# Kernel optimization log

Hardware: AMD Instinct MI355X
Metric: run time of the kernel (lower is better)

Reference implementation:

```python
import jax, jax.numpy as jnp
import numpy as np

CHANNELS = 32


def _mlp(x, W1, b1, W2, b2, W3, b3):
    # FNN: Linear -> ReLU -> Linear -> ReLU -> Linear (last layer linear)
    h = jax.nn.relu(x @ W1 + b1)
    h = jax.nn.relu(h @ W2 + b2)
    return h @ W3 + b3


def setup_inputs() -> dict:
    key = jax.random.key(0)
    ks = jax.random.split(key, 8)
    E = 262144
    C = CHANNELS
    H = 128
    d_in = 4  # 2 * spatial_dim
    d_out = C * (C + 1)  # 1056
    s = lambda fan_in: 1.0 / np.sqrt(fan_in)
    return {
        "pos_i": jax.random.normal(ks[0], (E, 2), jnp.float32),
        "pos_j": jax.random.normal(ks[1], (E, 2), jnp.float32),
        "v_j": jax.random.normal(ks[2], (E, C), jnp.float32),
        "W1": jax.random.normal(ks[3], (d_in, H), jnp.float32) * s(d_in),
        "b1": jnp.zeros((H,), jnp.float32),
        "W2": jax.random.normal(ks[4], (H, H), jnp.float32) * s(H),
        "b2": jnp.zeros((H,), jnp.float32),
        "W3": jax.random.normal(ks[5], (H, d_out), jnp.float32) * s(H),
        "b3": jnp.zeros((d_out,), jnp.float32),
    }


def reference(pos_i, pos_j, v_j, W1, b1, W2, b2, W3, b3):
    C = CHANNELS
    pos_ij = jnp.concatenate((pos_i, pos_j), axis=-1)          # [E, 2*spatial_dim]
    kernel = _mlp(pos_ij, W1, b1, W2, b2, W3, b3)
    kernel = kernel.reshape(-1, C, C + 1)                      # [E, C, C+1]
    mat, bias = kernel[..., :, :-1], kernel[..., :, -1]        # [E,C,C], [E,C]
    return jnp.einsum('eij,ej->ei', mat, v_j) + bias           # [E, C]
```

## Files before the change

### kernel.cpp

```cpp
#include <hip/hip_runtime.h>


#define E_TOTAL 262144
#define EPB 256
#define NBLK (E_TOTAL / EPB)

typedef float f32x4 __attribute__((ext_vector_type(4)));
typedef short s8v  __attribute__((ext_vector_type(8)));
typedef unsigned int u32;

__device__ __forceinline__ unsigned short f2bf(float x) {
  unsigned u = __float_as_uint(x);
  u += 0x7fffu + ((u >> 16) & 1u);
  return (unsigned short)(u >> 16);
}

__device__ __forceinline__ void ld16_g2l(const void* g, void* l) {
  __builtin_amdgcn_global_load_lds((const __attribute__((address_space(1))) u32*)g,
                                   (__attribute__((address_space(3))) u32*)l, 16, 0, 0);
}

__global__ void prep_pack(const float* __restrict__ W2, const float* __restrict__ W3,
                          const float* __restrict__ b3,
                          unsigned short* __restrict__ Wg2, unsigned short* __restrict__ W2f,
                          unsigned short* __restrict__ b3f, float* __restrict__ b3c) {
  int idx = blockIdx.x * 256 + threadIdx.x;
  if (idx < 135168) {
    int k = idx / 1056, c = idx % 1056;
    int i = c / 33, jc = c % 33;
    int col = jc * 32 + i;
    int nnt = col >> 4, low = col & 15;
    int nn = (nnt & 1) ? (33 + (nnt >> 1)) : (nnt >> 1);
    int ks = k >> 5, kr = k & 31;
    int lane = ((kr >> 3) << 4) + low;
    int jj = k & 7;
    Wg2[((nn * 4 + ks) * 64 + lane) * 8 + jj] = f2bf(W3[idx]);
  }
  if (idx < 16384) {
    int k = idx >> 7, n = idx & 127;
    int ks = k >> 5, kr = k & 31;
    int nt = n >> 4, low = n & 15;
    int l = ((kr >> 3) << 4) + low;
    int jj = k & 7;
    W2f[((ks * 8 + nt) * 64 + l) * 8 + jj] = f2bf(W2[idx]);
  }
  if (idx < 1024) {
    int jj = idx & 7, lane = (idx >> 3) & 63, ih = idx >> 9;
    int j = ((lane >> 4) << 3) + jj, i = ih * 16 + (lane & 15);
    b3f[idx] = f2bf(b3[i * 33 + j]);
  }
  if (idx < 32) b3c[idx] = b3[idx * 33 + 32];
}

__device__ __forceinline__ void tile_load(s8v (&dst)[4], const unsigned short* __restrict__ Wg2,
                                          int n, int lane) {
  const s8v* src = (const s8v*)(Wg2 + (size_t)n * 2048 + lane * 8);
#pragma unroll
  for (int ks = 0; ks < 4; ++ks) dst[ks] = src[ks * 64];
}

template <int IH>
__device__ __forceinline__ void tile_compute(const s8v (&bf)[4], const float* __restrict__ vt,
                                             int j, int eoff,
                                             const s8v (&af)[4][4], float (&oa)[2][4][4]) {
  const f32x4 zero4 = {0.f, 0.f, 0.f, 0.f};
  const float* vp = vt + j * 260 + eoff;
#pragma unroll
  for (int m = 0; m < 4; ++m) {
    f32x4 p = __builtin_amdgcn_mfma_f32_16x16x32_bf16(af[m][0], bf[0], zero4, 0, 0, 0);
#pragma unroll
    for (int ks = 1; ks < 4; ++ks)
      p = __builtin_amdgcn_mfma_f32_16x16x32_bf16(af[m][ks], bf[ks], p, 0, 0, 0);
    f32x4 vv = *(const f32x4*)(vp + m * 16);
#pragma unroll
    for (int r = 0; r < 4; ++r) oa[IH][m][r] += vv[r] * p[r];
  }
}

__global__ __launch_bounds__(256, 2) void fnn_fused(
    const float* __restrict__ pos_i, const float* __restrict__ pos_j,
    const float* __restrict__ vj, const float* __restrict__ W1,
    const float* __restrict__ b1, const float* __restrict__ b2,
    const unsigned short* __restrict__ W2f, const unsigned short* __restrict__ Wg2,
    const unsigned short* __restrict__ b3f, const float* __restrict__ b3c,
    float* __restrict__ out) {
  __shared__ __attribute__((aligned(16))) char smem[67584];
  float* vt = (float*)smem;
  unsigned short* h1c = (unsigned short*)smem;
  unsigned short* h2n = (unsigned short*)(smem + 17408);
  unsigned short* W2L = (unsigned short*)(smem + 34816);

  const int tid = threadIdx.x;
  const int w = tid >> 6, lane = tid & 63, q = lane >> 4, ln = lane & 15;
  const int B0 = blockIdx.x * EPB;
  const int eoff = w * 64 + q * 4;

  {
    const unsigned short* src = W2f + tid * 8;
    char* dstb = smem + 34816 + w * 1024;
#pragma unroll
    for (int cc = 0; cc < 8; ++cc)
      ld16_g2l(src + cc * 2048, dstb + cc * 4096);
  }

  float oa[2][4][4];
  {
    s8v av[4];
#pragma unroll
    for (int m = 0; m < 4; ++m) {
      int e = B0 + w * 64 + m * 16 + ln;
      const float4 va = *(const float4*)(vj + (size_t)e * 32 + q * 8);
      const float4 vb = *(const float4*)(vj + (size_t)e * 32 + q * 8 + 4);
      s8v t;
      t[0] = (short)f2bf(va.x); t[1] = (short)f2bf(va.y);
      t[2] = (short)f2bf(va.z); t[3] = (short)f2bf(va.w);
      t[4] = (short)f2bf(vb.x); t[5] = (short)f2bf(vb.y);
      t[6] = (short)f2bf(vb.z); t[7] = (short)f2bf(vb.w);
      av[m] = t;
    }
#pragma unroll
    for (int ih = 0; ih < 2; ++ih) {
      s8v b3fr = *(const s8v*)(b3f + (ih * 64 + lane) * 8);
      float cbv = b3c[ih * 16 + ln];
      f32x4 ci = {cbv, cbv, cbv, cbv};
#pragma unroll
      for (int m = 0; m < 4; ++m) {
        f32x4 p = __builtin_amdgcn_mfma_f32_16x16x32_bf16(av[m], b3fr, ci, 0, 0, 0);
#pragma unroll
        for (int r = 0; r < 4; ++r) oa[ih][m][r] = p[r];
      }
    }
  }

  const int hh0 = (tid & 15) * 8;
  float w1r[4][8], b1r[8], b2r[8];
#pragma unroll
  for (int d = 0; d < 4; ++d)
#pragma unroll
    for (int u = 0; u < 8; ++u) w1r[d][u] = W1[d * 128 + hh0 + u];
#pragma unroll
  for (int u = 0; u < 8; ++u) b1r[u] = b1[hh0 + u];
#pragma unroll
  for (int s = 0; s < 8; ++s) b2r[s] = b2[s * 16 + ln];

  s8v af[4][4];
  for (int qtr = 0; qtr < 4; ++qtr) {
#pragma unroll
    for (int half = 0; half < 4; ++half) {
      int ee = (tid >> 4) + half * 16;
      int eg = B0 + qtr * 64 + ee;
      float2 pi = *(const float2*)(pos_i + (size_t)eg * 2);
      float2 pj = *(const float2*)(pos_j + (size_t)eg * 2);
      s8v hv;
#pragma unroll
      for (int u = 0; u < 8; ++u) {
        float o = b1r[u] + pi.x * w1r[0][u] + pi.y * w1r[1][u] +
                  pj.x * w1r[2][u] + pj.y * w1r[3][u];
        hv[u] = (short)f2bf(fmaxf(o, 0.f));
      }
      *(s8v*)&h1c[ee * 136 + hh0] = hv;
    }
    __syncthreads();

#pragma unroll
    for (int s = 0; s < 8; ++s) {
      f32x4 a4 = {0.f, 0.f, 0.f, 0.f};
#pragma unroll
      for (int ks = 0; ks < 4; ++ks) {
        s8v afr = *(const s8v*)&h1c[(w * 16 + ln) * 136 + ks * 32 + q * 8];
        s8v bfr = *(const s8v*)&W2L[((ks * 8 + s) * 64 + lane) * 8];
        a4 = __builtin_amdgcn_mfma_f32_16x16x32_bf16(afr, bfr, a4, 0, 0, 0);
      }
      int eb = w * 16 + q * 4;
      int kc = s * 16 + ln;
#pragma unroll
      for (int r = 0; r < 4; ++r)
        h2n[(eb + r) * 136 + kc] = f2bf(fmaxf(a4[r] + b2r[s], 0.f));
    }
    __syncthreads();

    if (w == qtr) {
#pragma unroll
      for (int m = 0; m < 4; ++m)
#pragma unroll
        for (int ks = 0; ks < 4; ++ks)
          af[m][ks] = *(const s8v*)&h2n[(m * 16 + ln) * 136 + ks * 32 + q * 8];
    }
  }
  __syncthreads();

  s8v bf[4];
  tile_load(bf, Wg2, 0, lane);

  {
    const float* vrow = vj + (size_t)(B0 + tid) * 32;
#pragma unroll
    for (int j4 = 0; j4 < 8; ++j4) {
      float4 vv = *(const float4*)(vrow + j4 * 4);
      vt[(j4 * 4 + 0) * 260 + tid] = vv.x;
      vt[(j4 * 4 + 1) * 260 + tid] = vv.y;
      vt[(j4 * 4 + 2) * 260 + tid] = vv.z;
      vt[(j4 * 4 + 3) * 260 + tid] = vv.w;
    }
    vt[32 * 260 + tid] = 1.0f;
  }

#pragma unroll 1
  for (int n = 0; n < 33; ++n) {
    tile_compute<0>(bf, vt, n, eoff, af, oa);
    tile_load(bf, Wg2, n + 1, lane);
  }
#pragma unroll 1
  for (int n = 33; n < 66; ++n) {
    tile_compute<1>(bf, vt, n - 33, eoff, af, oa);
    tile_load(bf, Wg2, n + 1, lane);
  }

#pragma unroll
  for (int m = 0; m < 4; ++m)
#pragma unroll
    for (int ih = 0; ih < 2; ++ih)
#pragma unroll
      for (int r = 0; r < 4; ++r) {
        int e = B0 + w * 64 + m * 16 + q * 4 + r;
        out[(size_t)e * 32 + ih * 16 + ln] = oa[ih][m][r];
      }
}

extern "C" void kernel_launch(void* const* d_in, const int* in_sizes, int n_in,
                              void* d_out, int out_size, void* d_ws, size_t ws_size,
                              hipStream_t stream) {
  const float* pos_i = (const float*)d_in[0];
  const float* pos_j = (const float*)d_in[1];
  const float* vj    = (const float*)d_in[2];
  const float* W1    = (const float*)d_in[3];
  const float* b1    = (const float*)d_in[4];
  const float* W2    = (const float*)d_in[5];
  const float* b2    = (const float*)d_in[6];
  const float* W3    = (const float*)d_in[7];
  const float* b3    = (const float*)d_in[8];
  float* outp = (float*)d_out;

  unsigned short* Wg2 = (unsigned short*)d_ws;
  unsigned short* W2f = (unsigned short*)((char*)d_ws + 270336);
  unsigned short* b3f = (unsigned short*)((char*)d_ws + 303104);
  float*          b3c = (float*)((char*)d_ws + 305152);

  prep_pack<<<528, 256, 0, stream>>>(W2, W3, b3, Wg2, W2f, b3f, b3c);
  fnn_fused<<<NBLK, 256, 0, stream>>>(pos_i, pos_j, vj, W1, b1, b2, W2f, Wg2, b3f, b3c, outp);
}
```

Before: 176.6 us.

## Use 512-thread blocks with LDS double-buffered W3 tiles shared across waves

Blocks grow from 4 to 8 waves, and each wave now owns 32 edges instead of 64, which halves the accumulator and A-fragment registers per wave. W3 tiles are staged cooperatively into a double-buffered LDS region with global_load_lds plus a barrier per tile pair, replacing per-wave direct global loads. Layer 2 reads W2 fragments directly from global memory instead of from LDS. The intent is higher occupancy and less redundant global traffic for W3, at the cost of a __syncthreads per iteration and extra barrier stalls.

```diff
diff --git a/kernel.cpp b/kernel.cpp
--- a/kernel.cpp
+++ b/kernel.cpp
@@ -7,6 +7,7 @@
 
 typedef float f32x4 __attribute__((ext_vector_type(4)));
 typedef short s8v  __attribute__((ext_vector_type(8)));
+typedef short s4v  __attribute__((ext_vector_type(4)));
 typedef unsigned int u32;
 
 __device__ __forceinline__ unsigned short f2bf(float x) {
@@ -52,63 +53,116 @@
   if (idx < 32) b3c[idx] = b3[idx * 33 + 32];
 }
 
-__device__ __forceinline__ void tile_load(s8v (&dst)[4], const unsigned short* __restrict__ Wg2,
-                                          int n, int lane) {
-  const s8v* src = (const s8v*)(Wg2 + (size_t)n * 2048 + lane * 8);
-#pragma unroll
-  for (int ks = 0; ks < 4; ++ks) dst[ks] = src[ks * 64];
-}
-
 template <int IH>
-__device__ __forceinline__ void tile_compute(const s8v (&bf)[4], const float* __restrict__ vt,
-                                             int j, int eoff,
-                                             const s8v (&af)[4][4], float (&oa)[2][4][4]) {
+__device__ __forceinline__ void tile_compute(const unsigned short* __restrict__ buf, int t,
+                                             const float* __restrict__ vt, int j,
+                                             int w, int q, int lane,
+                                             const s8v (&af)[2][4], float (&oa)[2][2][4]) {
   const f32x4 zero4 = {0.f, 0.f, 0.f, 0.f};
-  const float* vp = vt + j * 260 + eoff;
-#pragma unroll
-  for (int m = 0; m < 4; ++m) {
-    f32x4 p = __builtin_amdgcn_mfma_f32_16x16x32_bf16(af[m][0], bf[0], zero4, 0, 0, 0);
+  s8v bfr[4];
+#pragma unroll
+  for (int ks = 0; ks < 4; ++ks)
+    bfr[ks] = *(const s8v*)&buf[(t * 4 + ks) * 512 + lane * 8];
+  const float* vp = vt + j * 260 + w * 32 + q * 4;
+#pragma unroll
+  for (int m = 0; m < 2; ++m) {
+    f32x4 p = __builtin_amdgcn_mfma_f32_16x16x32_bf16(af[m][0], bfr[0], zero4, 0, 0, 0);
 #pragma unroll
     for (int ks = 1; ks < 4; ++ks)
-      p = __builtin_amdgcn_mfma_f32_16x16x32_bf16(af[m][ks], bf[ks], p, 0, 0, 0);
+      p = __builtin_amdgcn_mfma_f32_16x16x32_bf16(af[m][ks], bfr[ks], p, 0, 0, 0);
     f32x4 vv = *(const f32x4*)(vp + m * 16);
 #pragma unroll
     for (int r = 0; r < 4; ++r) oa[IH][m][r] += vv[r] * p[r];
   }
 }
 
-__global__ __launch_bounds__(256, 2) void fnn_fused(
+__global__ __launch_bounds__(512, 4) void fnn_fused(
     const float* __restrict__ pos_i, const float* __restrict__ pos_j,
     const float* __restrict__ vj, const float* __restrict__ W1,
     const float* __restrict__ b1, const float* __restrict__ b2,
     const unsigned short* __restrict__ W2f, const unsigned short* __restrict__ Wg2,
     const unsigned short* __restrict__ b3f, const float* __restrict__ b3c,
     float* __restrict__ out) {
-  __shared__ __attribute__((aligned(16))) char smem[67584];
+  __shared__ __attribute__((aligned(16))) char smem[51200];
   float* vt = (float*)smem;
   unsigned short* h1c = (unsigned short*)smem;
   unsigned short* h2n = (unsigned short*)(smem + 17408);
-  unsigned short* W2L = (unsigned short*)(smem + 34816);
+  unsigned short* Bb  = (unsigned short*)(smem + 34816);
+  char* BbChar = smem + 34816;
 
   const int tid = threadIdx.x;
   const int w = tid >> 6, lane = tid & 63, q = lane >> 4, ln = lane & 15;
   const int B0 = blockIdx.x * EPB;
-  const int eoff = w * 64 + q * 4;
+
+  const int hh0 = (tid & 31) * 4;
+  float w1r[4][4], b1r4[4];
+#pragma unroll
+  for (int d = 0; d < 4; ++d)
+#pragma unroll
+    for (int u = 0; u < 4; ++u) w1r[d][u] = W1[d * 128 + hh0 + u];
+#pragma unroll
+  for (int u = 0; u < 4; ++u) b1r4[u] = b1[hh0 + u];
+
+  s8v af[2][4];
+  for (int qtr = 0; qtr < 4; ++qtr) {
+#pragma unroll
+    for (int half = 0; half < 4; ++half) {
+      int ee = (tid >> 5) + half * 16;
+      int eg = B0 + qtr * 64 + ee;
+      float2 pi = *(const float2*)(pos_i + (size_t)eg * 2);
+      float2 pj = *(const float2*)(pos_j + (size_t)eg * 2);
+      s4v hv;
+#pragma unroll
+      for (int u = 0; u < 4; ++u) {
+        float o = b1r4[u] + pi.x * w1r[0][u] + pi.y * w1r[1][u] +
+                  pj.x * w1r[2][u] + pj.y * w1r[3][u];
+        hv[u] = (short)f2bf(fmaxf(o, 0.f));
+      }
+      *(s4v*)&h1c[ee * 136 + hh0] = hv;
+    }
+    __syncthreads();
+
+#pragma unroll
+    for (int s = 0; s < 4; ++s) {
+      int tt = w * 4 + s, mt = tt >> 3, nt = tt & 7;
+      f32x4 a4 = {0.f, 0.f, 0.f, 0.f};
+#pragma unroll
+      for (int ks = 0; ks < 4; ++ks) {
+        s8v afr = *(const s8v*)&h1c[(mt * 16 + ln) * 136 + ks * 32 + q * 8];
+        s8v bfr = *(const s8v*)(W2f + ((ks * 8 + nt) * 64 + lane) * 8);
+        a4 = __builtin_amdgcn_mfma_f32_16x16x32_bf16(afr, bfr, a4, 0, 0, 0);
+      }
+      float b2v = b2[nt * 16 + ln];
+      int eb = mt * 16 + q * 4;
+      int kc = nt * 16 + ln;
+#pragma unroll
+      for (int r = 0; r < 4; ++r)
+        h2n[(eb + r) * 136 + kc] = f2bf(fmaxf(a4[r] + b2v, 0.f));
+    }
+    __syncthreads();
+
+    if ((w >> 1) == qtr) {
+#pragma unroll
+      for (int m = 0; m < 2; ++m)
+#pragma unroll
+        for (int ks = 0; ks < 4; ++ks)
+          af[m][ks] = *(const s8v*)&h2n[(((w & 1) * 32 + m * 16 + ln)) * 136 + ks * 32 + q * 8];
+    }
+  }
 
   {
-    const unsigned short* src = W2f + tid * 8;
-    char* dstb = smem + 34816 + w * 1024;
-#pragma unroll
-    for (int cc = 0; cc < 8; ++cc)
-      ld16_g2l(src + cc * 2048, dstb + cc * 4096);
-  }
-
-  float oa[2][4][4];
+    const unsigned short* src = Wg2 + tid * 8;
+    char* dstb = BbChar + w * 1024;
+    ld16_g2l(src, dstb);
+  }
+  __syncthreads();
+
+  float oa[2][2][4];
   {
-    s8v av[4];
-#pragma unroll
-    for (int m = 0; m < 4; ++m) {
-      int e = B0 + w * 64 + m * 16 + ln;
+    s8v av[2];
+#pragma unroll
+    for (int m = 0; m < 2; ++m) {
+      int e = B0 + w * 32 + m * 16 + ln;
       const float4 va = *(const float4*)(vj + (size_t)e * 32 + q * 8);
       const float4 vb = *(const float4*)(vj + (size_t)e * 32 + q * 8 + 4);
       s8v t;
@@ -124,7 +178,7 @@
       float cbv = b3c[ih * 16 + ln];
       f32x4 ci = {cbv, cbv, cbv, cbv};
 #pragma unroll
-      for (int m = 0; m < 4; ++m) {
+      for (int m = 0; m < 2; ++m) {
         f32x4 p = __builtin_amdgcn_mfma_f32_16x16x32_bf16(av[m], b3fr, ci, 0, 0, 0);
 #pragma unroll
         for (int r = 0; r < 4; ++r) oa[ih][m][r] = p[r];
@@ -132,67 +186,7 @@
     }
   }
 
-  const int hh0 = (tid & 15) * 8;
-  float w1r[4][8], b1r[8], b2r[8];
-#pragma unroll
-  for (int d = 0; d < 4; ++d)
-#pragma unroll
-    for (int u = 0; u < 8; ++u) w1r[d][u] = W1[d * 128 + hh0 + u];
-#pragma unroll
-  for (int u = 0; u < 8; ++u) b1r[u] = b1[hh0 + u];
-#pragma unroll
-  for (int s = 0; s < 8; ++s) b2r[s] = b2[s * 16 + ln];
-
-  s8v af[4][4];
-  for (int qtr = 0; qtr < 4; ++qtr) {
-#pragma unroll
-    for (int half = 0; half < 4; ++half) {
-      int ee = (tid >> 4) + half * 16;
-      int eg = B0 + qtr * 64 + ee;
-      float2 pi = *(const float2*)(pos_i + (size_t)eg * 2);
-      float2 pj = *(const float2*)(pos_j + (size_t)eg * 2);
-      s8v hv;
-#pragma unroll
-      for (int u = 0; u < 8; ++u) {
-        float o = b1r[u] + pi.x * w1r[0][u] + pi.y * w1r[1][u] +
-                  pj.x * w1r[2][u] + pj.y * w1r[3][u];
-        hv[u] = (short)f2bf(fmaxf(o, 0.f));
-      }
-      *(s8v*)&h1c[ee * 136 + hh0] = hv;
-    }
-    __syncthreads();
-
-#pragma unroll
-    for (int s = 0; s < 8; ++s) {
-      f32x4 a4 = {0.f, 0.f, 0.f, 0.f};
-#pragma unroll
-      for (int ks = 0; ks < 4; ++ks) {
-        s8v afr = *(const s8v*)&h1c[(w * 16 + ln) * 136 + ks * 32 + q * 8];
-        s8v bfr = *(const s8v*)&W2L[((ks * 8 + s) * 64 + lane) * 8];
-        a4 = __builtin_amdgcn_mfma_f32_16x16x32_bf16(afr, bfr, a4, 0, 0, 0);
-      }
-      int eb = w * 16 + q * 4;
-      int kc = s * 16 + ln;
-#pragma unroll
-      for (int r = 0; r < 4; ++r)
-        h2n[(eb + r) * 136 + kc] = f2bf(fmaxf(a4[r] + b2r[s], 0.f));
-    }
-    __syncthreads();
-
-    if (w == qtr) {
-#pragma unroll
-      for (int m = 0; m < 4; ++m)
-#pragma unroll
-        for (int ks = 0; ks < 4; ++ks)
-          af[m][ks] = *(const s8v*)&h2n[(m * 16 + ln) * 136 + ks * 32 + q * 8];
-    }
-  }
-  __syncthreads();
-
-  s8v bf[4];
-  tile_load(bf, Wg2, 0, lane);
-
-  {
+  if (tid < 256) {
     const float* vrow = vj + (size_t)(B0 + tid) * 32;
 #pragma unroll
     for (int j4 = 0; j4 < 8; ++j4) {
@@ -204,25 +198,51 @@
     }
     vt[32 * 260 + tid] = 1.0f;
   }
+  __syncthreads();
 
 #pragma unroll 1
-  for (int n = 0; n < 33; ++n) {
-    tile_compute<0>(bf, vt, n, eoff, af, oa);
-    tile_load(bf, Wg2, n + 1, lane);
+  for (int c = 0; c < 16; ++c) {
+    const unsigned short* buf = Bb + (c & 1) * 4096;
+    {
+      const unsigned short* src = Wg2 + (size_t)(c + 1) * 4096 + tid * 8;
+      char* dstb = BbChar + ((c + 1) & 1) * 8192 + w * 1024;
+      ld16_g2l(src, dstb);
+    }
+    tile_compute<0>(buf, 0, vt, 2 * c,     w, q, lane, af, oa);
+    tile_compute<0>(buf, 1, vt, 2 * c + 1, w, q, lane, af, oa);
+    __syncthreads();
+  }
+  {
+    const unsigned short* buf = Bb;
+    {
+      const unsigned short* src = Wg2 + (size_t)17 * 4096 + tid * 8;
+      char* dstb = BbChar + 8192 + w * 1024;
+      ld16_g2l(src, dstb);
+    }
+    tile_compute<0>(buf, 0, vt, 32, w, q, lane, af, oa);
+    tile_compute<1>(buf, 1, vt, 0,  w, q, lane, af, oa);
+    __syncthreads();
   }
 #pragma unroll 1
-  for (int n = 33; n < 66; ++n) {
-    tile_compute<1>(bf, vt, n - 33, eoff, af, oa);
-    tile_load(bf, Wg2, n + 1, lane);
-  }
-
-#pragma unroll
-  for (int m = 0; m < 4; ++m)
+  for (int c = 17; c < 33; ++c) {
+    const unsigned short* buf = Bb + (c & 1) * 4096;
+    if (c < 32) {
+      const unsigned short* src = Wg2 + (size_t)(c + 1) * 4096 + tid * 8;
+      char* dstb = BbChar + ((c + 1) & 1) * 8192 + w * 1024;
+      ld16_g2l(src, dstb);
+    }
+    tile_compute<1>(buf, 0, vt, 2 * c - 33, w, q, lane, af, oa);
+    tile_compute<1>(buf, 1, vt, 2 * c - 32, w, q, lane, af, oa);
+    __syncthreads();
+  }
+
+#pragma unroll
+  for (int m = 0; m < 2; ++m)
 #pragma unroll
     for (int ih = 0; ih < 2; ++ih)
 #pragma unroll
       for (int r = 0; r < 4; ++r) {
-        int e = B0 + w * 64 + m * 16 + q * 4 + r;
+        int e = B0 + w * 32 + m * 16 + q * 4 + r;
         out[(size_t)e * 32 + ih * 16 + ln] = oa[ih][m][r];
       }
 }
@@ -247,5 +267,5 @@
   float*          b3c = (float*)((char*)d_ws + 305152);
 
   prep_pack<<<528, 256, 0, stream>>>(W2, W3, b3, Wg2, W2f, b3f, b3c);
-  fnn_fused<<<NBLK, 256, 0, stream>>>(pos_i, pos_j, vj, W1, b1, b2, W2f, Wg2, b3f, b3c, outp);
-}
+  fnn_fused<<<NBLK, 512, 0, stream>>>(pos_i, pos_j, vj, W1, b1, b2, W2f, Wg2, b3f, b3c, outp);
+}
```

Result: slower. 205.7 us (+16.5%).

## Split fused kernel into h2 pass and generation pass via workspace fragments

Applied to the files above, without the earlier changes.

Splits the single fused kernel into two kernels. The first computes layers 1 and 2 for 64 edges per block and writes the h2 activations to workspace in MFMA fragment layout. The second reads those fragments and runs the W3 contraction with smaller LDS, which could allow higher occupancy. The aim is to remove the serial per-quarter MLP phase and its barriers from the heavy kernel, at the cost of about 64 MB of extra global traffic and one more launch. The split only runs when the workspace is large enough; otherwise the fused kernel is kept, with a barrier moved inside its loop.

```diff
diff --git a/kernel.cpp b/kernel.cpp
--- a/kernel.cpp
+++ b/kernel.cpp
@@ -4,9 +4,11 @@
 #define E_TOTAL 262144
 #define EPB 256
 #define NBLK (E_TOTAL / EPB)
+#define NEED_WS (524288ull + 67108864ull)
 
 typedef float f32x4 __attribute__((ext_vector_type(4)));
 typedef short s8v  __attribute__((ext_vector_type(8)));
+typedef short s4v  __attribute__((ext_vector_type(4)));
 typedef unsigned int u32;
 
 __device__ __forceinline__ unsigned short f2bf(float x) {
@@ -52,6 +54,76 @@
   if (idx < 32) b3c[idx] = b3[idx * 33 + 32];
 }
 
+__global__ __launch_bounds__(256, 3) void h2_pass(
+    const float* __restrict__ pos_i, const float* __restrict__ pos_j,
+    const float* __restrict__ W1, const float* __restrict__ b1,
+    const float* __restrict__ b2, const unsigned short* __restrict__ W2f,
+    unsigned short* __restrict__ h2frag) {
+  __shared__ __attribute__((aligned(16))) char smem[34816];
+  unsigned short* h1c = (unsigned short*)smem;
+  unsigned short* h2n = (unsigned short*)(smem + 17408);
+
+  const int tid = threadIdx.x;
+  const int w = tid >> 6, lane = tid & 63, q = lane >> 4, ln = lane & 15;
+  const int B0h = blockIdx.x * 64;
+
+  const int hh0 = (tid & 31) * 4;
+  float w1r[4][4], b1r4[4], b2r[8];
+#pragma unroll
+  for (int d = 0; d < 4; ++d)
+#pragma unroll
+    for (int u = 0; u < 4; ++u) w1r[d][u] = W1[d * 128 + hh0 + u];
+#pragma unroll
+  for (int u = 0; u < 4; ++u) b1r4[u] = b1[hh0 + u];
+#pragma unroll
+  for (int s = 0; s < 8; ++s) b2r[s] = b2[s * 16 + ln];
+
+#pragma unroll
+  for (int half = 0; half < 8; ++half) {
+    int ee = (tid >> 5) + half * 8;
+    int eg = B0h + ee;
+    float2 pi = *(const float2*)(pos_i + (size_t)eg * 2);
+    float2 pj = *(const float2*)(pos_j + (size_t)eg * 2);
+    s4v hv;
+#pragma unroll
+    for (int u = 0; u < 4; ++u) {
+      float o = b1r4[u] + pi.x * w1r[0][u] + pi.y * w1r[1][u] +
+                pj.x * w1r[2][u] + pj.y * w1r[3][u];
+      hv[u] = (short)f2bf(fmaxf(o, 0.f));
+    }
+    *(s4v*)&h1c[ee * 136 + hh0] = hv;
+  }
+  __syncthreads();
+
+#pragma unroll
+  for (int s = 0; s < 8; ++s) {
+    f32x4 a4 = {0.f, 0.f, 0.f, 0.f};
+#pragma unroll
+    for (int ks = 0; ks < 4; ++ks) {
+      s8v afr = *(const s8v*)&h1c[(w * 16 + ln) * 136 + ks * 32 + q * 8];
+      s8v bfr = *(const s8v*)(W2f + ((ks * 8 + s) * 64 + lane) * 8);
+      a4 = __builtin_amdgcn_mfma_f32_16x16x32_bf16(afr, bfr, a4, 0, 0, 0);
+    }
+    int eb = w * 16 + q * 4;
+    int kc = s * 16 + ln;
+#pragma unroll
+    for (int r = 0; r < 4; ++r)
+      h2n[(eb + r) * 136 + kc] = f2bf(fmaxf(a4[r] + b2r[s], 0.f));
+  }
+  __syncthreads();
+
+  {
+    int f = tid >> 4, g = f >> 2, ks = f & 3, s = tid & 15;
+    unsigned short* dst = h2frag + ((size_t)(blockIdx.x * 16 + f)) * 512;
+#pragma unroll
+    for (int r4 = 0; r4 < 4; ++r4) {
+      int l = s * 4 + r4;
+      s8v v = *(const s8v*)&h2n[(g * 16 + (l & 15)) * 136 + ks * 32 + (l >> 4) * 8];
+      *(s8v*)&dst[l * 8] = v;
+    }
+  }
+}
+
 __device__ __forceinline__ void tile_load(s8v (&dst)[4], const unsigned short* __restrict__ Wg2,
                                           int n, int lane) {
   const s8v* src = (const s8v*)(Wg2 + (size_t)n * 2048 + lane * 8);
@@ -75,6 +147,92 @@
 #pragma unroll
     for (int r = 0; r < 4; ++r) oa[IH][m][r] += vv[r] * p[r];
   }
+}
+
+__global__ __launch_bounds__(256, 2) void g_pass(
+    const float* __restrict__ vj, const unsigned short* __restrict__ Wg2,
+    const unsigned short* __restrict__ b3f, const float* __restrict__ b3c,
+    const unsigned short* __restrict__ h2frag, float* __restrict__ out) {
+  __shared__ __attribute__((aligned(16))) char smem[34320];
+  float* vt = (float*)smem;
+
+  const int tid = threadIdx.x;
+  const int w = tid >> 6, lane = tid & 63, q = lane >> 4, ln = lane & 15;
+  const int B0 = blockIdx.x * EPB;
+  const int eoff = w * 64 + q * 4;
+
+  s8v af[4][4];
+#pragma unroll
+  for (int m = 0; m < 4; ++m)
+#pragma unroll
+    for (int ks = 0; ks < 4; ++ks)
+      af[m][ks] = *(const s8v*)&h2frag[((size_t)(blockIdx.x * 16 + w * 4 + m) * 4 + ks) * 512 + lane * 8];
+
+  float oa[2][4][4];
+  {
+    s8v av[4];
+#pragma unroll
+    for (int m = 0; m < 4; ++m) {
+      int e = B0 + w * 64 + m * 16 + ln;
+      const float4 va = *(const float4*)(vj + (size_t)e * 32 + q * 8);
+      const float4 vb = *(const float4*)(vj + (size_t)e * 32 + q * 8 + 4);
+      s8v t;
+      t[0] = (short)f2bf(va.x); t[1] = (short)f2bf(va.y);
+      t[2] = (short)f2bf(va.z); t[3] = (short)f2bf(va.w);
+      t[4] = (short)f2bf(vb.x); t[5] = (short)f2bf(vb.y);
+      t[6] = (short)f2bf(vb.z); t[7] = (short)f2bf(vb.w);
+      av[m] = t;
+    }
+#pragma unroll
+    for (int ih = 0; ih < 2; ++ih) {
+      s8v b3fr = *(const s8v*)(b3f + (ih * 64 + lane) * 8);
+      float cbv = b3c[ih * 16 + ln];
+      f32x4 ci = {cbv, cbv, cbv, cbv};
+#pragma unroll
+      for (int m = 0; m < 4; ++m) {
+        f32x4 p = __builtin_amdgcn_mfma_f32_16x16x32_bf16(av[m], b3fr, ci, 0, 0, 0);
+#pragma unroll
+        for (int r = 0; r < 4; ++r) oa[ih][m][r] = p[r];
+      }
+    }
+  }
+
+  s8v bf[4];
+  tile_load(bf, Wg2, 0, lane);
+
+  {
+    const float* vrow = vj + (size_t)(B0 + tid) * 32;
+#pragma unroll
+    for (int j4 = 0; j4 < 8; ++j4) {
+      float4 vv = *(const float4*)(vrow + j4 * 4);
+      vt[(j4 * 4 + 0) * 260 + tid] = vv.x;
+      vt[(j4 * 4 + 1) * 260 + tid] = vv.y;
+      vt[(j4 * 4 + 2) * 260 + tid] = vv.z;
+      vt[(j4 * 4 + 3) * 260 + tid] = vv.w;
+    }
+    vt[32 * 260 + tid] = 1.0f;
+  }
+
+#pragma unroll 1
+  for (int n = 0; n < 33; ++n) {
+    tile_compute<0>(bf, vt, n, eoff, af, oa);
+    tile_load(bf, Wg2, n + 1, lane);
+  }
+#pragma unroll 1
+  for (int n = 33; n < 66; ++n) {
+    tile_compute<1>(bf, vt, n - 33, eoff, af, oa);
+    tile_load(bf, Wg2, n + 1, lane);
+  }
+
+#pragma unroll
+  for (int m = 0; m < 4; ++m)
+#pragma unroll
+    for (int ih = 0; ih < 2; ++ih)
+#pragma unroll
+      for (int r = 0; r < 4; ++r) {
+        int e = B0 + w * 64 + m * 16 + q * 4 + r;
+        out[(size_t)e * 32 + ih * 16 + ln] = oa[ih][m][r];
+      }
 }
 
 __global__ __launch_bounds__(256, 2) void fnn_fused(
@@ -161,7 +319,6 @@
       *(s8v*)&h1c[ee * 136 + hh0] = hv;
     }
     __syncthreads();
-
 #pragma unroll
     for (int s = 0; s < 8; ++s) {
       f32x4 a4 = {0.f, 0.f, 0.f, 0.f};
@@ -178,7 +335,6 @@
         h2n[(eb + r) * 136 + kc] = f2bf(fmaxf(a4[r] + b2r[s], 0.f));
     }
     __syncthreads();
-
     if (w == qtr) {
 #pragma unroll
       for (int m = 0; m < 4; ++m)
@@ -186,8 +342,8 @@
         for (int ks = 0; ks < 4; ++ks)
           af[m][ks] = *(const s8v*)&h2n[(m * 16 + ln) * 136 + ks * 32 + q * 8];
     }
-  }
-  __syncthreads();
+    __syncthreads();
+  }
 
   s8v bf[4];
   tile_load(bf, Wg2, 0, lane);
@@ -245,7 +401,13 @@
   unsigned short* W2f = (unsigned short*)((char*)d_ws + 270336);
   unsigned short* b3f = (unsigned short*)((char*)d_ws + 303104);
   float*          b3c = (float*)((char*)d_ws + 305152);
+  unsigned short* h2frag = (unsigned short*)((char*)d_ws + 524288);
 
   prep_pack<<<528, 256, 0, stream>>>(W2, W3, b3, Wg2, W2f, b3f, b3c);
-  fnn_fused<<<NBLK, 256, 0, stream>>>(pos_i, pos_j, vj, W1, b1, b2, W2f, Wg2, b3f, b3c, outp);
-}
+  if (ws_size >= NEED_WS) {
+    h2_pass<<<E_TOTAL / 64, 256, 0, stream>>>(pos_i, pos_j, W1, b1, b2, W2f, h2frag);
+    g_pass<<<NBLK, 256, 0, stream>>>(vj, Wg2, b3f, b3c, h2frag, outp);
+  } else {
+    fnn_fused<<<NBLK, 256, 0, stream>>>(pos_i, pos_j, vj, W1, b1, b2, W2f, Wg2, b3f, b3c, outp);
+  }
+}
```

Result: slower. 202.5 us (+14.7%).
